# Kernel tuning notes

Measured on AMD Instinct MI355X. Metric: run time of the kernel, lower is better.

## Reference

```python
import jax, jax.numpy as jnp
import numpy as np

COMMITMENT_COST = 0.25


def setup_inputs() -> dict:
    key = jax.random.key(0)
    kx, kc = jax.random.split(key)
    x = jax.random.normal(kx, (8, 32768, 8), dtype=jnp.float32)
    codebooks = jax.random.normal(kc, (8, 1024, 8), dtype=jnp.float32)  # [Q, K, D]
    return {"x": x, "codebooks": codebooks}


def reference(x, codebooks):
    # x: [B, T, D]; codebooks: [Q, K, D]
    residual = x
    quantized = jnp.zeros_like(x)
    loss = jnp.float32(0.0)
    codes = []
    num_q = codebooks.shape[0]
    for q in range(num_q):
        cb = codebooks[q]  # [K, D]
        # squared L2 distances: ||r||^2 + ||c||^2 - 2 r.c  -> [B, T, K]
        dist = (
            jnp.sum(residual * residual, axis=-1, keepdims=True)
            + jnp.sum(cb * cb, axis=-1)
            - 2.0 * jnp.einsum("btd,kd->btk", residual, cb)
        )
        idx = jnp.argmin(dist, axis=-1)  # [B, T]
        codes.append(idx)
        emb = cb[idx]  # [B, T, D] gather
        quantized = quantized + emb
        residual = residual - emb
        loss = loss + jnp.mean((jax.lax.stop_gradient(residual) - emb) ** 2)
    # straight-through estimator
    quantized = x + jax.lax.stop_gradient(quantized - x)
    return quantized, loss * COMMITMENT_COST, jnp.stack(codes)  # codes: [Q, B, T]
```

## Files before the change

### kernel.cpp

```cpp
#include <hip/hip_runtime.h>


#define TOKENS   262144
#define D        8
#define K        1024
#define Q        8
#define LOSS_OFF 2097152
#define CODES_OFF 2097153

#define BLK      256
#define GRID     (TOKENS / BLK)

__device__ __forceinline__ float np_sum8_pureseq(const float* __restrict__ p) {
#pragma clang fp contract(off)
  float s = p[0];
  s = s + p[1]; s = s + p[2]; s = s + p[3]; s = s + p[4];
  s = s + p[5]; s = s + p[6]; s = s + p[7];
  return s;
}

__global__ __launch_bounds__(BLK) void rvq_prep(const float* __restrict__ cb,
                                                float* __restrict__ cc) {
#pragma clang fp contract(off)
  int i = blockIdx.x * BLK + threadIdx.x;
  const float* c = cb + i * D;
  float p[D];
#pragma unroll
  for (int d = 0; d < D; ++d) p[d] = c[d] * c[d];
  cc[i] = np_sum8_pureseq(p);
}

__global__ __launch_bounds__(BLK) void rvq_main(const float* __restrict__ x,
                                                const float* __restrict__ cb,
                                                const float* __restrict__ cct,
                                                float* __restrict__ out,
                                                double* __restrict__ partials) {
#pragma clang fp contract(off)
  __shared__ float sC[K][D];
  __shared__ float sCC[K];
  const int tid = threadIdx.x;
  const int bt = blockIdx.x * BLK + tid;

  float rf[D];
  float qv[D];
  {
    const float4* xp = (const float4*)(x + bt * D);
    float4 a = xp[0], b = xp[1];
    rf[0] = a.x; rf[1] = a.y; rf[2] = a.z; rf[3] = a.w;
    rf[4] = b.x; rf[5] = b.y; rf[6] = b.z; rf[7] = b.w;
#pragma unroll
    for (int d = 0; d < D; ++d) qv[d] = 0.0f;
  }
  double lossAcc = 0.0;

  for (int q = 0; q < Q; ++q) {
    __syncthreads();
    {
      const float4* src = (const float4*)(cb + q * (K * D));
      float4* dst = (float4*)sC;
      for (int i = tid; i < (K * D) / 4; i += BLK) dst[i] = src[i];
      const float* ccq = cct + q * K;
      for (int i = tid; i < K; i += BLK) sCC[i] = ccq[i];
    }
    __syncthreads();

    float rr;
    {
      float p[D];
#pragma unroll
      for (int d = 0; d < D; ++d) p[d] = rf[d] * rf[d];
      rr = np_sum8_pureseq(p);
    }

    float best = 3.402823466e+38f;
    int idx = 0;
#pragma unroll 4
    for (int k = 0; k < K; ++k) {
      const float4* row = (const float4*)sC[k];
      float4 ca = row[0], cb4 = row[1];
      float ccv = sCC[k];

      float m0 = rf[0] * ca.x, m1 = rf[1] * ca.y, m2 = rf[2] * ca.z,
            m3 = rf[3] * ca.w, m4 = rf[4] * cb4.x, m5 = rf[5] * cb4.y,
            m6 = rf[6] * cb4.z, m7 = rf[7] * cb4.w;
      float l0 = m0 + m4, l1 = m1 + m5, l2 = m2 + m6, l3 = m3 + m7;
      float dot = (l0 + l1) + (l2 + l3);
      float s = (rr + ccv) - 2.0f * dot;
      if (s < best) { best = s; idx = k; }
    }

#pragma unroll
    for (int d = 0; d < D; ++d) {
      float e = sC[idx][d];
      qv[d] = qv[d] + e;
      rf[d] = rf[d] - e;
      float f = rf[d] - e;
      lossAcc = fma((double)f, (double)f, lossAcc);
    }
    out[CODES_OFF + q * TOKENS + bt] = (float)idx;
  }

  {
    const float4* xp = (const float4*)(x + bt * D);
    float4 a = xp[0], b = xp[1];
    float xs[D];
    xs[0] = a.x; xs[1] = a.y; xs[2] = a.z; xs[3] = a.w;
    xs[4] = b.x; xs[5] = b.y; xs[6] = b.z; xs[7] = b.w;
    float o[D];
#pragma unroll
    for (int d = 0; d < D; ++d) o[d] = xs[d] + (qv[d] - xs[d]);
    float4 v;
    v.x = o[0]; v.y = o[1]; v.z = o[2]; v.w = o[3];
    ((float4*)(out + bt * D))[0] = v;
    v.x = o[4]; v.y = o[5]; v.z = o[6]; v.w = o[7];
    ((float4*)(out + bt * D))[1] = v;
  }

  for (int off = 32; off; off >>= 1) lossAcc += __shfl_down(lossAcc, off);
  __syncthreads();
  double* red = (double*)sC;
  if ((tid & 63) == 0) red[tid >> 6] = lossAcc;
  __syncthreads();
  if (tid == 0) partials[blockIdx.x] = red[0] + red[1] + red[2] + red[3];
}

__global__ __launch_bounds__(BLK) void rvq_loss(const double* __restrict__ partials,
                                                float* __restrict__ out) {
  int tid = threadIdx.x;
  double s = partials[tid] + partials[tid + BLK] +
             partials[tid + 2 * BLK] + partials[tid + 3 * BLK];
  for (int off = 32; off; off >>= 1) s += __shfl_down(s, off);
  __shared__ double red[4];
  if ((tid & 63) == 0) red[tid >> 6] = s;
  __syncthreads();
  if (tid == 0)
    out[LOSS_OFF] = (float)((red[0] + red[1] + red[2] + red[3]) *
                            (0.25 / 2097152.0));
}

extern "C" void kernel_launch(void* const* d_in, const int* in_sizes, int n_in,
                              void* d_out, int out_size, void* d_ws, size_t ws_size,
                              hipStream_t stream) {
  const float* x  = (const float*)d_in[0];
  const float* cb = (const float*)d_in[1];
  float* out = (float*)d_out;
  double* partials = (double*)d_ws;
  float* cc = (float*)(partials + GRID);

  rvq_prep<<<(Q * K) / BLK, BLK, 0, stream>>>(cb, cc);
  rvq_main<<<GRID, BLK, 0, stream>>>(x, cb, cc, out, partials);
  rvq_loss<<<1, BLK, 0, stream>>>(partials, out);
}
```

Before: 1.074 ms.

## Pack two tokens per lane with packed fp32 math and split codebook across half-waves

Each wave now handles 64 tokens, but every lane processes two tokens at once using 2-wide float vectors, so the compiler can emit packed FP32 multiply/add instructions. The two half-waves each scan half of the codebook, and a cross-lane shuffle merges their best distances with a tie-break that keeps the lower index. This aims to halve the per-token shared-memory codebook reads and roughly halve the ALU instruction count in the argmin loop. The cost is extra shuffles and select logic per stage, and half the lanes sit idle during the loss and output writes.

```diff
diff --git a/kernel.cpp b/kernel.cpp
--- a/kernel.cpp
+++ b/kernel.cpp
@@ -10,6 +10,8 @@
 
 #define BLK      256
 #define GRID     (TOKENS / BLK)
+
+typedef float v2f __attribute__((ext_vector_type(2)));
 
 __device__ __forceinline__ float np_sum8_pureseq(const float* __restrict__ p) {
 #pragma clang fp contract(off)
@@ -38,18 +40,27 @@
 #pragma clang fp contract(off)
   __shared__ float sC[K][D];
   __shared__ float sCC[K];
-  const int tid = threadIdx.x;
-  const int bt = blockIdx.x * BLK + tid;
-
-  float rf[D];
-  float qv[D];
+  const int tid  = threadIdx.x;
+  const int wid  = tid >> 6;
+  const int lane = tid & 63;
+  const int half = lane >> 5;
+  const int sub  = lane & 31;
+  const int t0 = blockIdx.x * 256 + wid * 64 + sub;
+  const int t1 = t0 + 32;
+  const int kb = half * (K / 2);
+
+  v2f rf2[D];
+  v2f qv2[D];
   {
-    const float4* xp = (const float4*)(x + bt * D);
-    float4 a = xp[0], b = xp[1];
-    rf[0] = a.x; rf[1] = a.y; rf[2] = a.z; rf[3] = a.w;
-    rf[4] = b.x; rf[5] = b.y; rf[6] = b.z; rf[7] = b.w;
-#pragma unroll
-    for (int d = 0; d < D; ++d) qv[d] = 0.0f;
+    const float4* xa = (const float4*)(x + t0 * D);
+    const float4* xb = (const float4*)(x + t1 * D);
+    float4 a0 = xa[0], a1 = xa[1], b0 = xb[0], b1 = xb[1];
+    rf2[0] = (v2f){a0.x, b0.x}; rf2[1] = (v2f){a0.y, b0.y};
+    rf2[2] = (v2f){a0.z, b0.z}; rf2[3] = (v2f){a0.w, b0.w};
+    rf2[4] = (v2f){a1.x, b1.x}; rf2[5] = (v2f){a1.y, b1.y};
+    rf2[6] = (v2f){a1.z, b1.z}; rf2[7] = (v2f){a1.w, b1.w};
+#pragma unroll
+    for (int d = 0; d < D; ++d) qv2[d] = (v2f){0.0f, 0.0f};
   }
   double lossAcc = 0.0;
 
@@ -64,56 +75,92 @@
     }
     __syncthreads();
 
-    float rr;
+    v2f rr2;
     {
-      float p[D];
-#pragma unroll
-      for (int d = 0; d < D; ++d) p[d] = rf[d] * rf[d];
-      rr = np_sum8_pureseq(p);
-    }
-
-    float best = 3.402823466e+38f;
-    int idx = 0;
+      v2f p[D];
+#pragma unroll
+      for (int d = 0; d < D; ++d) p[d] = rf2[d] * rf2[d];
+      v2f s = p[0];
+      s = s + p[1]; s = s + p[2]; s = s + p[3]; s = s + p[4];
+      s = s + p[5]; s = s + p[6]; s = s + p[7];
+      rr2 = s;
+    }
+
+    const float* cbase = &sC[kb][0];
+    const float* ccb   = &sCC[kb];
+    float bestA = 3.402823466e+38f, bestB = 3.402823466e+38f;
+    int ia = kb, ib = kb;
 #pragma unroll 4
-    for (int k = 0; k < K; ++k) {
-      const float4* row = (const float4*)sC[k];
+    for (int k = 0; k < K / 2; ++k) {
+      const float4* row = (const float4*)(cbase + k * D);
       float4 ca = row[0], cb4 = row[1];
-      float ccv = sCC[k];
-
-      float m0 = rf[0] * ca.x, m1 = rf[1] * ca.y, m2 = rf[2] * ca.z,
-            m3 = rf[3] * ca.w, m4 = rf[4] * cb4.x, m5 = rf[5] * cb4.y,
-            m6 = rf[6] * cb4.z, m7 = rf[7] * cb4.w;
-      float l0 = m0 + m4, l1 = m1 + m5, l2 = m2 + m6, l3 = m3 + m7;
-      float dot = (l0 + l1) + (l2 + l3);
-      float s = (rr + ccv) - 2.0f * dot;
-      if (s < best) { best = s; idx = k; }
-    }
+      float ccv = ccb[k];
+
+      v2f m0 = rf2[0] * ca.x,  m1 = rf2[1] * ca.y,
+          m2 = rf2[2] * ca.z,  m3 = rf2[3] * ca.w,
+          m4 = rf2[4] * cb4.x, m5 = rf2[5] * cb4.y,
+          m6 = rf2[6] * cb4.z, m7 = rf2[7] * cb4.w;
+      v2f l0 = m0 + m4, l1 = m1 + m5, l2 = m2 + m6, l3 = m3 + m7;
+      v2f dot = (l0 + l1) + (l2 + l3);
+      v2f u = rr2 + ccv;
+      v2f s = u - (dot + dot);
+      if (s.x < bestA) { bestA = s.x; ia = kb + k; }
+      if (s.y < bestB) { bestB = s.y; ib = kb + k; }
+    }
+
+    float obA = __shfl_xor(bestA, 32);
+    float obB = __shfl_xor(bestB, 32);
+    int   oiA = __shfl_xor(ia, 32);
+    int   oiB = __shfl_xor(ib, 32);
+    float loA = half ? obA : bestA,  hiA = half ? bestA : obA;
+    int   liA = half ? oiA : ia,     hiiA = half ? ia : oiA;
+    int idxA = (loA <= hiA) ? liA : hiiA;
+    float loB = half ? obB : bestB,  hiB = half ? bestB : obB;
+    int   liB = half ? oiB : ib,     hiiB = half ? ib : oiB;
+    int idxB = (loB <= hiB) ? liB : hiiB;
 
 #pragma unroll
     for (int d = 0; d < D; ++d) {
-      float e = sC[idx][d];
-      qv[d] = qv[d] + e;
-      rf[d] = rf[d] - e;
-      float f = rf[d] - e;
-      lossAcc = fma((double)f, (double)f, lossAcc);
-    }
-    out[CODES_OFF + q * TOKENS + bt] = (float)idx;
+      float eA = sC[idxA][d];
+      float qA = qv2[d].x + eA; qv2[d].x = qA;
+      float rA = rf2[d].x - eA; rf2[d].x = rA;
+      float fA = rA - eA;
+      float eB = sC[idxB][d];
+      float qB = qv2[d].y + eB; qv2[d].y = qB;
+      float rB = rf2[d].y - eB; rf2[d].y = rB;
+      float fB = rB - eB;
+      if (!half) {
+        lossAcc = fma((double)fA, (double)fA, lossAcc);
+        lossAcc = fma((double)fB, (double)fB, lossAcc);
+      }
+    }
+    if (!half) {
+      out[CODES_OFF + q * TOKENS + t0] = (float)idxA;
+      out[CODES_OFF + q * TOKENS + t1] = (float)idxB;
+    }
   }
 
-  {
-    const float4* xp = (const float4*)(x + bt * D);
-    float4 a = xp[0], b = xp[1];
-    float xs[D];
-    xs[0] = a.x; xs[1] = a.y; xs[2] = a.z; xs[3] = a.w;
-    xs[4] = b.x; xs[5] = b.y; xs[6] = b.z; xs[7] = b.w;
-    float o[D];
-#pragma unroll
-    for (int d = 0; d < D; ++d) o[d] = xs[d] + (qv[d] - xs[d]);
+  if (!half) {
+    const float4* xa = (const float4*)(x + t0 * D);
+    const float4* xb = (const float4*)(x + t1 * D);
+    float4 a0 = xa[0], a1 = xa[1], b0 = xb[0], b1 = xb[1];
+    float xsA[D] = {a0.x, a0.y, a0.z, a0.w, a1.x, a1.y, a1.z, a1.w};
+    float xsB[D] = {b0.x, b0.y, b0.z, b0.w, b1.x, b1.y, b1.z, b1.w};
+    float oA[D], oB[D];
+#pragma unroll
+    for (int d = 0; d < D; ++d) {
+      oA[d] = xsA[d] + (qv2[d].x - xsA[d]);
+      oB[d] = xsB[d] + (qv2[d].y - xsB[d]);
+    }
     float4 v;
-    v.x = o[0]; v.y = o[1]; v.z = o[2]; v.w = o[3];
-    ((float4*)(out + bt * D))[0] = v;
-    v.x = o[4]; v.y = o[5]; v.z = o[6]; v.w = o[7];
-    ((float4*)(out + bt * D))[1] = v;
+    v.x = oA[0]; v.y = oA[1]; v.z = oA[2]; v.w = oA[3];
+    ((float4*)(out + t0 * D))[0] = v;
+    v.x = oA[4]; v.y = oA[5]; v.z = oA[6]; v.w = oA[7];
+    ((float4*)(out + t0 * D))[1] = v;
+    v.x = oB[0]; v.y = oB[1]; v.z = oB[2]; v.w = oB[3];
+    ((float4*)(out + t1 * D))[0] = v;
+    v.x = oB[4]; v.y = oB[5]; v.z = oB[6]; v.w = oB[7];
+    ((float4*)(out + t1 * D))[1] = v;
   }
 
   for (int off = 32; off; off >>= 1) lossAcc += __shfl_down(lossAcc, off);
```

Measured after the change: 927.8 us. 1.16x faster.
